# Kernel optimization log

Hardware: AMD Instinct MI355X
Metric: run time of the kernel (lower is better)

Reference implementation:

```python
import jax, jax.numpy as jnp
import numpy as np

N_NODES = 50000
N_EDGES = 800000
IN_CH, HID_CH, OUT_CH = 128, 256, 128


def _glorot(key, shape):
    fan_in, fan_out = shape[1], shape[0]
    lim = float(np.sqrt(6.0 / (fan_in + fan_out)))
    return jax.random.uniform(key, shape, jnp.float32, -lim, lim)


def setup_inputs() -> dict:
    key = jax.random.key(0)
    ks = jax.random.split(key, 8)
    x = jax.random.normal(ks[0], (N_NODES, IN_CH), jnp.float32)
    edge_index = jax.random.randint(ks[1], (2, N_EDGES), 0, N_NODES, jnp.int64)
    return {
        "x": x,
        "edge_index": edge_index,
        # layer 1: SAGEConv(128 -> 256): lin_l (with bias) on aggregated, lin_r (no bias) on root
        "W1l": _glorot(ks[2], (HID_CH, IN_CH)),
        "b1l": jnp.zeros((HID_CH,), jnp.float32),
        "W1r": _glorot(ks[3], (HID_CH, IN_CH)),
        # layer 2: SAGEConv(256 -> 128)
        "W2l": _glorot(ks[4], (OUT_CH, HID_CH)),
        "b2l": jnp.zeros((OUT_CH,), jnp.float32),
        "W2r": _glorot(ks[5], (OUT_CH, HID_CH)),
    }


def _sage_conv(x, src, dst, Wl, bl, Wr, n_nodes):
    # mean-aggregate neighbor (source) features at destination nodes
    msg = x[src]                                                   # [E, C] gather
    agg = jax.ops.segment_sum(msg, dst, num_segments=n_nodes)      # [N, C]
    deg = jax.ops.segment_sum(jnp.ones((src.shape[0],), x.dtype), dst,
                              num_segments=n_nodes)                # [N]
    mean = agg / jnp.maximum(deg, 1.0)[:, None]                    # zero-degree -> 0
    return mean @ Wl.T + bl + x @ Wr.T


def reference(x, edge_index, W1l, b1l, W1r, W2l, b2l, W2r):
    src, dst = edge_index[0], edge_index[1]
    n = x.shape[0]
    h = _sage_conv(x, src, dst, W1l, b1l, W1r, n)
    h = jax.nn.relu(h)  # dropout is identity in eval mode
    out = _sage_conv(h, src, dst, W2l, b2l, W2r, n)
    return out
```

## Files before the change

### kernel.cpp

```cpp
#include <hip/hip_runtime.h>

#define N_NODES 50000
#define IN_CH   128
#define HID_CH  256
#define OUT_CH  128

#define NB    196
#define NWG   256
#define NBNW  (NB * NWG)

#define XBLK  3125
#define WBLK  64

typedef __attribute__((ext_vector_type(8))) short bf16x8;
typedef __attribute__((ext_vector_type(4))) float f32x4;
typedef __attribute__((ext_vector_type(2))) float f32x2;

__device__ __forceinline__ unsigned short f32_bf16_rne(float f) {
    unsigned u = __float_as_uint(f);
    unsigned r = u + 0x7fff + ((u >> 16) & 1);
    return (unsigned short)(r >> 16);
}

__device__ __forceinline__ void cvt8_io(const float* __restrict__ inp,
                                        unsigned short* __restrict__ outp)
{
    const float4* p = reinterpret_cast<const float4*>(inp);
    float4 a = p[0], b = p[1];
    alignas(16) unsigned short t[8] = {
        f32_bf16_rne(a.x), f32_bf16_rne(a.y), f32_bf16_rne(a.z), f32_bf16_rne(a.w),
        f32_bf16_rne(b.x), f32_bf16_rne(b.y), f32_bf16_rne(b.z), f32_bf16_rne(b.w)};
    *reinterpret_cast<int4*>(outp) = *reinterpret_cast<const int4*>(t);
}

__global__ __launch_bounds__(256) void prep_kernel(
    const int* __restrict__ src, const int* __restrict__ dst,
    int* __restrict__ counts, int E, int chunk,
    const float* __restrict__ x, unsigned short* __restrict__ A1,
    unsigned char* __restrict__ xb8,
    const float* __restrict__ W1l, const float* __restrict__ W1r,
    const float* __restrict__ W2l, const float* __restrict__ W2r,
    unsigned short* __restrict__ B1, unsigned short* __restrict__ W2cat)
{
    const int b = blockIdx.x;
    if (b < NWG) {
        __shared__ int h[NB];
        for (int i = threadIdx.x; i < NB; i += 256) h[i] = 0;
        __syncthreads();
        const int e0 = b * chunk;
        const int e1 = min(e0 + chunk, E);
        for (int e = e0 + threadIdx.x; e < e1; e += 256) {
            int s = src[e], d = dst[e];
            if ((unsigned)s < (unsigned)N_NODES && (unsigned)d < (unsigned)N_NODES)
                atomicAdd(&h[d >> 8], 1);
        }
        __syncthreads();
        for (int i = threadIdx.x; i < NB; i += 256)
            counts[i * NWG + b] = h[i];
    } else if (b < NWG + XBLK) {
        size_t j = (size_t)(b - NWG) * 256 + threadIdx.x;
        const float4* p = reinterpret_cast<const float4*>(x) + 2 * j;
        float4 a = p[0], bb = p[1];
        alignas(16) unsigned short t[8] = {
            f32_bf16_rne(a.x),  f32_bf16_rne(a.y),  f32_bf16_rne(a.z),  f32_bf16_rne(a.w),
            f32_bf16_rne(bb.x), f32_bf16_rne(bb.y), f32_bf16_rne(bb.z), f32_bf16_rne(bb.w)};
        const size_t node = j >> 4, chunk16 = j & 15;
        *reinterpret_cast<int4*>(A1 + node * 256 + 128 + chunk16 * 8) =
            *reinterpret_cast<const int4*>(t);
        unsigned u0 = __builtin_amdgcn_cvt_pk_fp8_f32(a.x, a.y, 0, false);
        u0 = __builtin_amdgcn_cvt_pk_fp8_f32(a.z, a.w, u0, true);
        unsigned u1 = __builtin_amdgcn_cvt_pk_fp8_f32(bb.x, bb.y, 0, false);
        u1 = __builtin_amdgcn_cvt_pk_fp8_f32(bb.z, bb.w, u1, true);
        uint2 uv; uv.x = u0; uv.y = u1;
        *reinterpret_cast<uint2*>(xb8 + 8 * j) = uv;
    } else {
        int idx = (b - NWG - XBLK) * 256 + threadIdx.x;
        int seg = idx >> 12, j = idx & 4095;
        if (seg == 0) {
            int row = j >> 4, cb = (j & 15) * 8;
            cvt8_io(W1l + (size_t)j * 8, B1 + (size_t)row * 256 + cb);
        } else if (seg == 1) {
            int row = j >> 4, cb = (j & 15) * 8;
            cvt8_io(W1r + (size_t)j * 8, B1 + (size_t)row * 256 + 128 + cb);
        } else if (seg == 2) {
            int row = j >> 5, cb = (j & 31) * 8;
            cvt8_io(W2l + (size_t)j * 8, W2cat + (size_t)row * 256 + cb);
        } else {
            int row = j >> 5, cb = (j & 31) * 8;
            cvt8_io(W2r + (size_t)j * 8, W2cat + (size_t)(128 + row) * 256 + cb);
        }
    }
}

__global__ __launch_bounds__(256) void scan_kernel(
    const int* __restrict__ counts, int* __restrict__ S)
{
    __shared__ int red[256];
    const int t = threadIdx.x;
    const int b = blockIdx.x;
    const int lim = b * NWG;
    int partial = 0;
    for (int i = t; i < lim; i += 256) partial += counts[i];
    red[t] = partial;
    __syncthreads();
    for (int off = 128; off >= 1; off >>= 1) {
        if (t < off) red[t] += red[t + off];
        __syncthreads();
    }
    const int base_b = red[0];
    __syncthreads();
    const int v = counts[b * NWG + t];
    red[t] = v;
    __syncthreads();
    for (int off = 1; off < 256; off <<= 1) {
        int u = (t >= off) ? red[t - off] : 0;
        __syncthreads();
        if (t >= off) red[t] += u;
        __syncthreads();
    }
    S[b * NWG + t] = base_b + red[t] - v;
    if (b == NB - 1 && t == 255) S[NBNW] = base_b + red[255];
}

__global__ __launch_bounds__(256) void bscatter_kernel(
    const int* __restrict__ src, const int* __restrict__ dst,
    const int* __restrict__ S, int* __restrict__ pairs, int E, int chunk)
{
    __shared__ int cur[NB];
    const int w = blockIdx.x;
    for (int i = threadIdx.x; i < NB; i += 256) cur[i] = S[i * NWG + w];
    __syncthreads();
    const int e0 = w * chunk;
    const int e1 = min(e0 + chunk, E);
    for (int e = e0 + threadIdx.x; e < e1; e += 256) {
        int s = src[e], d = dst[e];
        if ((unsigned)s < (unsigned)N_NODES && (unsigned)d < (unsigned)N_NODES) {
            int pos = atomicAdd(&cur[d >> 8], 1);
            pairs[pos] = (s << 8) | (d & 255);
        }
    }
}

__global__ __launch_bounds__(256) void bsort_kernel(
    const int* __restrict__ pairs, const int* __restrict__ S,
    int* __restrict__ rowptr, int* __restrict__ colidx)
{
    __shared__ int hcnt[256];
    __shared__ int hcur[256];
    const int b = blockIdx.x;
    const int start = S[b * NWG];
    const int endv  = (b == NB - 1) ? S[NBNW] : S[(b + 1) * NWG];

    hcnt[threadIdx.x] = 0;
    __syncthreads();
    for (int e = start + threadIdx.x; e < endv; e += 256)
        atomicAdd(&hcnt[pairs[e] & 255], 1);
    __syncthreads();
    for (int off = 1; off < 256; off <<= 1) {
        int t = (threadIdx.x >= off) ? hcnt[threadIdx.x - off] : 0;
        __syncthreads();
        if (threadIdx.x >= off) hcnt[threadIdx.x] += t;
        __syncthreads();
    }
    int offv = (threadIdx.x == 0) ? 0 : hcnt[threadIdx.x - 1];
    hcur[threadIdx.x] = offv;
    int node = (b << 8) + threadIdx.x;
    if (node < N_NODES) rowptr[node] = start + offv;
    if (b == NB - 1 && threadIdx.x == 0) rowptr[N_NODES] = endv;
    __syncthreads();
    for (int e = start + threadIdx.x; e < endv; e += 256) {
        int p = pairs[e];
        int pos = atomicAdd(&hcur[p & 255], 1);
        colidx[start + pos] = (unsigned)p >> 8;
    }
}

#define ACC16(v)                                                             \
    { f32x2 a0 = __builtin_amdgcn_cvt_pk_f32_fp8(v.x, false);                \
      f32x2 a1 = __builtin_amdgcn_cvt_pk_f32_fp8(v.x, true);                 \
      f32x2 a2 = __builtin_amdgcn_cvt_pk_f32_fp8(v.y, false);                \
      f32x2 a3 = __builtin_amdgcn_cvt_pk_f32_fp8(v.y, true);                 \
      f32x2 a4 = __builtin_amdgcn_cvt_pk_f32_fp8(v.z, false);                \
      f32x2 a5 = __builtin_amdgcn_cvt_pk_f32_fp8(v.z, true);                 \
      f32x2 a6 = __builtin_amdgcn_cvt_pk_f32_fp8(v.w, false);                \
      f32x2 a7 = __builtin_amdgcn_cvt_pk_f32_fp8(v.w, true);                 \
      acc[0]  += a0.x; acc[1]  += a0.y; acc[2]  += a1.x; acc[3]  += a1.y;    \
      acc[4]  += a2.x; acc[5]  += a2.y; acc[6]  += a3.x; acc[7]  += a3.y;    \
      acc[8]  += a4.x; acc[9]  += a4.y; acc[10] += a5.x; acc[11] += a5.y;    \
      acc[12] += a6.x; acc[13] += a6.y; acc[14] += a7.x; acc[15] += a7.y; }

#define LDROW16(s, CH) (*reinterpret_cast<const uint4*>(feat + (size_t)(s) * (CH) + c16))

#define AGG_BODY(CH)                                                            \
    const int node = blockIdx.x * 16 + (threadIdx.x >> 4);                      \
    if (node >= N_NODES) return;                                                \
    const int l8 = threadIdx.x & 15;                                            \
    const int half = l8 >> 3;                  \
    const int c16 = (l8 & 7) * 16;                   \
    const int beg = rowptr[node], end = rowptr[node + 1];                       \
    const int len = end - beg;                                                  \
    float acc[16] = {};                                                         \
    for (int base = beg; base < end; base += 16) {                              \
        const int cnt = min(16, end - base);                                    \
        int ci = colidx[base + ((l8 < cnt) ? l8 : 0)];                          \
        int k = 0;                                                              \
        for (; k + 7 < cnt; k += 8) {                                           \
            int s0 = __shfl(ci, k + half,     16);                              \
            int s1 = __shfl(ci, k + half + 2, 16);                              \
            int s2 = __shfl(ci, k + half + 4, 16);                              \
            int s3 = __shfl(ci, k + half + 6, 16);                              \
            uint4 v0 = LDROW16(s0, CH); uint4 v1 = LDROW16(s1, CH);             \
            uint4 v2 = LDROW16(s2, CH); uint4 v3 = LDROW16(s3, CH);             \
            ACC16(v0) ACC16(v1) ACC16(v2) ACC16(v3)                             \
        }                                                                       \
        for (; k < cnt; k += 2) {                                               \
            int e = k + half;                                                   \
            int s0 = __shfl(ci, (e < cnt) ? e : 0, 16);                         \
            if (e < cnt) { uint4 v0 = LDROW16(s0, CH); ACC16(v0) }              \
        }                                                                       \
    }                                                                           \
    _Pragma("unroll")                                                           \
    for (int q = 0; q < 16; ++q) acc[q] += __shfl_xor(acc[q], 8);               \
    float accw[8];                                                              \
    _Pragma("unroll")                                                           \
    for (int q = 0; q < 8; ++q) accw[q] = half ? acc[q + 8] : acc[q];           \
    const int cb = c16 + half * 8;            \
    const float sc = 1.0f / fmaxf((float)len, 1.0f);

__global__ __launch_bounds__(256) void agg1_kernel(
    const unsigned char* __restrict__ feat, const int* __restrict__ rowptr,
    const int* __restrict__ colidx, unsigned short* __restrict__ A1)
{
    AGG_BODY(IN_CH)
    alignas(16) unsigned short t[8];
#pragma unroll
    for (int q = 0; q < 8; ++q) t[q] = f32_bf16_rne(accw[q] * sc);
    *reinterpret_cast<int4*>(A1 + (size_t)node * 256 + cb) =
        *reinterpret_cast<const int4*>(t);
}

__global__ __launch_bounds__(256) void agg2_kernel(
    const unsigned char* __restrict__ feat, const int* __restrict__ rowptr,
    const int* __restrict__ colidx, const unsigned short* __restrict__ hrb,
    const float* __restrict__ b2l, float* __restrict__ out)
{
    AGG_BODY(OUT_CH)
    const int4 hv = *reinterpret_cast<const int4*>(hrb + (size_t)node * OUT_CH + cb);
    const unsigned short* hs = reinterpret_cast<const unsigned short*>(&hv);
    float4 b0 = *reinterpret_cast<const float4*>(b2l + cb);
    float4 b1 = *reinterpret_cast<const float4*>(b2l + cb + 4);
    float4 o0, o1;
    o0.x = accw[0] * sc + __uint_as_float((unsigned)hs[0] << 16) + b0.x;
    o0.y = accw[1] * sc + __uint_as_float((unsigned)hs[1] << 16) + b0.y;
    o0.z = accw[2] * sc + __uint_as_float((unsigned)hs[2] << 16) + b0.z;
    o0.w = accw[3] * sc + __uint_as_float((unsigned)hs[3] << 16) + b0.w;
    o1.x = accw[4] * sc + __uint_as_float((unsigned)hs[4] << 16) + b1.x;
    o1.y = accw[5] * sc + __uint_as_float((unsigned)hs[5] << 16) + b1.y;
    o1.z = accw[6] * sc + __uint_as_float((unsigned)hs[6] << 16) + b1.z;
    o1.w = accw[7] * sc + __uint_as_float((unsigned)hs[7] << 16) + b1.w;
    float* o = out + (size_t)node * OUT_CH + cb;
    reinterpret_cast<float4*>(o)[0] = o0;
    reinterpret_cast<float4*>(o)[1] = o1;
}

template <int NIT>
__device__ __forceinline__ void stage8(
    const unsigned short* __restrict__ g, int ldg, int rowBase, int maxRow,
    int kBase, unsigned short* __restrict__ s, int tid)
{
    const int wave = tid >> 6;
    const int lane = tid & 63;
    const int r_in = lane >> 3;
    const int c_g  = (lane & 7) ^ r_in;
#pragma unroll
    for (int it = 0; it < NIT; ++it) {
        const int rowBlk = it * 64 + wave * 8;
        int row = rowBase + rowBlk + r_in;
        if (row >= maxRow) row = maxRow - 1;
        const unsigned short* gp = g + (size_t)row * ldg + kBase + c_g * 8;
        unsigned short* lp = s + rowBlk * 64;
        __builtin_amdgcn_global_load_lds(
            (const __attribute__((address_space(1))) unsigned int*)gp,
            (__attribute__((address_space(3))) unsigned int*)lp,
            16, 0, 0);
    }
}

__device__ __forceinline__ const bf16x8* frag_ptr(
    const unsigned short* __restrict__ s, int rr, int c)
{
    return reinterpret_cast<const bf16x8*>(s + rr * 64 + (((c ^ (rr & 7))) << 3));
}

__device__ __forceinline__ const bf16x8* hfrag_ptr(
    const unsigned short* __restrict__ s, int rr, int kbc, int c)
{
    return reinterpret_cast<const bf16x8*>(
        s + rr * 256 + ((kbc + (c ^ (rr & 7))) << 3));
}

__device__ __forceinline__ void mfma_tile(
    const unsigned short* __restrict__ As, const unsigned short* __restrict__ Bs,
    int wm, int wn, int l16, int quad, f32x4 acc[4][4])
{
#pragma unroll
    for (int k0 = 0; k0 < 64; k0 += 32) {
        const int c = (k0 >> 3) + quad;
        bf16x8 a[4], b[4];
#pragma unroll
        for (int i = 0; i < 4; ++i)
            a[i] = *frag_ptr(As, wm * 64 + i * 16 + l16, c);
#pragma unroll
        for (int j = 0; j < 4; ++j)
            b[j] = *frag_ptr(Bs, wn * 64 + j * 16 + l16, c);
#pragma unroll
        for (int i = 0; i < 4; ++i)
#pragma unroll
            for (int j = 0; j < 4; ++j)
                acc[i][j] = __builtin_amdgcn_mfma_f32_16x16x32_bf16(
                    b[j], a[i], acc[i][j], 0, 0, 0);
    }
}

__device__ __forceinline__ void mfma_tile_h(
    const unsigned short* __restrict__ Hs, const unsigned short* __restrict__ Bs,
    int kbc, int wm, int wn, int l16, int quad, f32x4 acc[4][4])
{
#pragma unroll
    for (int k0 = 0; k0 < 64; k0 += 32) {
        const int c = (k0 >> 3) + quad;
        bf16x8 a[4], b[4];
#pragma unroll
        for (int i = 0; i < 4; ++i)
            a[i] = *hfrag_ptr(Hs, wm * 64 + i * 16 + l16, kbc, c);
#pragma unroll
        for (int j = 0; j < 4; ++j)
            b[j] = *frag_ptr(Bs, wn * 64 + j * 16 + l16, c);
#pragma unroll
        for (int i = 0; i < 4; ++i)
#pragma unroll
            for (int j = 0; j < 4; ++j)
                acc[i][j] = __builtin_amdgcn_mfma_f32_16x16x32_bf16(
                    b[j], a[i], acc[i][j], 0, 0, 0);
    }
}

__global__ __launch_bounds__(512) void gemm_fused(
    const unsigned short* __restrict__ A1, const unsigned short* __restrict__ B1,
    const float* __restrict__ b1l, const unsigned short* __restrict__ W2cat,
    unsigned char* __restrict__ pb8, unsigned short* __restrict__ hrb)
{
    __shared__ unsigned short As[128 * 64];
    __shared__ unsigned short Bs[256 * 64];
    __shared__ unsigned short Hs[128 * 256];
    const int tid = threadIdx.x;
    const int wid = tid >> 6, lane = tid & 63;
    const int wm = wid & 1, wn = wid >> 1;
    const int l16 = lane & 15, quad = lane >> 4;
    const int rowBase = blockIdx.x * 128;

    f32x4 z = {0.f, 0.f, 0.f, 0.f};
    f32x4 acc[4][4];
#pragma unroll
    for (int i = 0; i < 4; ++i)
#pragma unroll
        for (int j = 0; j < 4; ++j) acc[i][j] = z;

#pragma unroll
    for (int kb = 0; kb < 256; kb += 64) {
        __syncthreads();
        stage8<2>(A1, 256, rowBase, N_NODES, kb, As, tid);
        stage8<4>(B1, 256, 0, HID_CH, kb, Bs, tid);
        __syncthreads();
        mfma_tile(As, Bs, wm, wn, l16, quad, acc);
    }

#pragma unroll
    for (int i = 0; i < 4; ++i) {
        const int rr = wm * 64 + i * 16 + l16;
#pragma unroll
        for (int j = 0; j < 4; ++j) {
            const int colBase = wn * 64 + j * 16 + quad * 4;
            float4 bv = *reinterpret_cast<const float4*>(b1l + colBase);
            alignas(8) unsigned short t[4];
            t[0] = f32_bf16_rne(fmaxf(acc[i][j][0] + bv.x, 0.0f));
            t[1] = f32_bf16_rne(fmaxf(acc[i][j][1] + bv.y, 0.0f));
            t[2] = f32_bf16_rne(fmaxf(acc[i][j][2] + bv.z, 0.0f));
            t[3] = f32_bf16_rne(fmaxf(acc[i][j][3] + bv.w, 0.0f));
            const int grp  = colBase >> 6;
            const int lc   = (colBase >> 3) & 7;
            const int half = (colBase >> 2) & 1;
            unsigned short* hp = Hs + rr * 256 +
                (((grp << 3) + (lc ^ (rr & 7))) << 3) + half * 4;
            *reinterpret_cast<uint2*>(hp) = *reinterpret_cast<const uint2*>(t);
        }
    }

#pragma unroll
    for (int i = 0; i < 4; ++i)
#pragma unroll
        for (int j = 0; j < 4; ++j) acc[i][j] = z;

#pragma unroll
    for (int kb = 0; kb < HID_CH; kb += 64) {
        __syncthreads();
        stage8<4>(W2cat, HID_CH, 0, 256, kb, Bs, tid);
        __syncthreads();
        mfma_tile_h(Hs, Bs, kb >> 3, wm, wn, l16, quad, acc);
    }

    if (wn < 2) {
#pragma unroll
        for (int i = 0; i < 4; ++i) {
            int m = rowBase + wm * 64 + i * 16 + l16;
            if (m >= N_NODES) continue;
#pragma unroll
            for (int j = 0; j < 4; ++j) {
                int col = wn * 64 + j * 16 + quad * 4;
                unsigned u = __builtin_amdgcn_cvt_pk_fp8_f32(
                    acc[i][j][0], acc[i][j][1], 0, false);
                u = __builtin_amdgcn_cvt_pk_fp8_f32(
                    acc[i][j][2], acc[i][j][3], u, true);
                *reinterpret_cast<unsigned*>(pb8 + (size_t)m * OUT_CH + col) = u;
            }
        }
    } else {
#pragma unroll
        for (int i = 0; i < 4; ++i) {
            int m = rowBase + wm * 64 + i * 16 + l16;
            if (m >= N_NODES) continue;
#pragma unroll
            for (int j = 0; j < 4; ++j) {
                int col = wn * 64 + j * 16 + quad * 4 - 128;
                alignas(8) unsigned short t[4];
                t[0] = f32_bf16_rne(acc[i][j][0]);
                t[1] = f32_bf16_rne(acc[i][j][1]);
                t[2] = f32_bf16_rne(acc[i][j][2]);
                t[3] = f32_bf16_rne(acc[i][j][3]);
                *reinterpret_cast<uint2*>(hrb + (size_t)m * OUT_CH + col) =
                    *reinterpret_cast<const uint2*>(t);
            }
        }
    }
}

extern "C" void kernel_launch(void* const* d_in, const int* in_sizes, int n_in,
                              void* d_out, int out_size, void* d_ws, size_t ws_size,
                              hipStream_t stream)
{
    const float* x   = (const float*)d_in[0];
    const int*   ei  = (const int*)d_in[1];
    const float* W1l = (const float*)d_in[2];
    const float* b1l = (const float*)d_in[3];
    const float* W1r = (const float*)d_in[4];
    const float* W2l = (const float*)d_in[5];
    const float* b2l = (const float*)d_in[6];
    const float* W2r = (const float*)d_in[7];

    const int E = in_sizes[1] / 2;
    const int* src = ei;
    const int* dst = ei + E;

    char* ws = (char*)d_ws;
    size_t off = 0;
    auto alloc = [&](size_t bytes) {
        void* p = ws + off;
        off += (bytes + 255) & ~(size_t)255;
        return p;
    };
    unsigned short* A1     = (unsigned short*)alloc((size_t)N_NODES * 256 * 2);
    unsigned char*  xb8    = (unsigned char*)alloc((size_t)N_NODES * IN_CH);
    unsigned char*  pb8    = (unsigned char*)alloc((size_t)N_NODES * OUT_CH);
    unsigned short* hrb    = (unsigned short*)alloc((size_t)N_NODES * OUT_CH * 2);
    unsigned short* B1     = (unsigned short*)alloc((size_t)HID_CH * 256 * 2);
    unsigned short* W2cat  = (unsigned short*)alloc((size_t)256 * HID_CH * 2);
    int* counts = (int*)alloc((size_t)NBNW * 4);
    int* S      = (int*)alloc((size_t)(NBNW + 1) * 4);
    int* pairs  = (int*)alloc((size_t)E * 4);
    int* rowptr = (int*)alloc((size_t)(N_NODES + 1) * 4);
    int* colidx = (int*)alloc((size_t)E * 4);
    float* out = (float*)d_out;

    const int chunk = (E + NWG - 1) / NWG;

    prep_kernel<<<NWG + XBLK + WBLK, 256, 0, stream>>>(
        src, dst, counts, E, chunk, x, A1, xb8,
        W1l, W1r, W2l, W2r, B1, W2cat);
    scan_kernel<<<NB, 256, 0, stream>>>(counts, S);
    bscatter_kernel<<<NWG, 256, 0, stream>>>(src, dst, S, pairs, E, chunk);
    bsort_kernel<<<NB, 256, 0, stream>>>(pairs, S, rowptr, colidx);

    const int aggBlocks = (N_NODES + 15) / 16;
    const int mBlocks = (N_NODES + 127) / 128;

    agg1_kernel<<<aggBlocks, 256, 0, stream>>>(xb8, rowptr, colidx, A1);
    gemm_fused<<<mBlocks, 512, 0, stream>>>(A1, B1, b1l, W2cat, pb8, hrb);
    agg2_kernel<<<aggBlocks, 256, 0, stream>>>(pb8, rowptr, colidx, hrb, b2l, out);
}
```

Before: 263.6 us.

## Use 8 lanes per node in aggregation with 8-edge unrolled gathers

The neighbor aggregation kernels now assign 8 lanes per node instead of 16. Each lane covers all 16 fp8 channels of a 16-byte chunk and processes every edge, rather than splitting edges across two half-groups. This removes the cross-half shuffle reduction and doubles the number of nodes per block. It also unrolls 8 independent row gathers per iteration to keep more loads in flight. In exchange, each lane does twice the serial accumulation work per node, which may lengthen latency for high-degree nodes.

```diff
diff --git a/kernel.cpp b/kernel.cpp
--- a/kernel.cpp
+++ b/kernel.cpp
@@ -189,54 +189,59 @@
       acc[8]  += a4.x; acc[9]  += a4.y; acc[10] += a5.x; acc[11] += a5.y;    \
       acc[12] += a6.x; acc[13] += a6.y; acc[14] += a7.x; acc[15] += a7.y; }
 
-#define LDROW16(s, CH) (*reinterpret_cast<const uint4*>(feat + (size_t)(s) * (CH) + c16))
-
-#define AGG_BODY(CH)                                                            \
-    const int node = blockIdx.x * 16 + (threadIdx.x >> 4);                      \
-    if (node >= N_NODES) return;                                                \
-    const int l8 = threadIdx.x & 15;                                            \
-    const int half = l8 >> 3;                  \
-    const int c16 = (l8 & 7) * 16;                   \
-    const int beg = rowptr[node], end = rowptr[node + 1];                       \
-    const int len = end - beg;                                                  \
+#define LDROW16(s, CH) (*reinterpret_cast<const uint4*>(feat + (size_t)(s) * (CH) + l8 * 16))
+
+#define AGG_LOOP(CH)                                                            \
     float acc[16] = {};                                                         \
-    for (int base = beg; base < end; base += 16) {                              \
-        const int cnt = min(16, end - base);                                    \
+    for (int base = beg; base < end; base += 8) {                               \
+        const int cnt = min(8, end - base);                                     \
         int ci = colidx[base + ((l8 < cnt) ? l8 : 0)];                          \
-        int k = 0;                                                              \
-        for (; k + 7 < cnt; k += 8) {                                           \
-            int s0 = __shfl(ci, k + half,     16);                              \
-            int s1 = __shfl(ci, k + half + 2, 16);                              \
-            int s2 = __shfl(ci, k + half + 4, 16);                              \
-            int s3 = __shfl(ci, k + half + 6, 16);                              \
+        if (cnt == 8) {                                                         \
+            int s0 = __shfl(ci, 0, 8), s1 = __shfl(ci, 1, 8);                   \
+            int s2 = __shfl(ci, 2, 8), s3 = __shfl(ci, 3, 8);                   \
+            int s4 = __shfl(ci, 4, 8), s5 = __shfl(ci, 5, 8);                   \
+            int s6 = __shfl(ci, 6, 8), s7 = __shfl(ci, 7, 8);                   \
             uint4 v0 = LDROW16(s0, CH); uint4 v1 = LDROW16(s1, CH);             \
             uint4 v2 = LDROW16(s2, CH); uint4 v3 = LDROW16(s3, CH);             \
+            uint4 v4 = LDROW16(s4, CH); uint4 v5 = LDROW16(s5, CH);             \
+            uint4 v6 = LDROW16(s6, CH); uint4 v7 = LDROW16(s7, CH);             \
             ACC16(v0) ACC16(v1) ACC16(v2) ACC16(v3)                             \
-        }                                                                       \
-        for (; k < cnt; k += 2) {                                               \
-            int e = k + half;                                                   \
-            int s0 = __shfl(ci, (e < cnt) ? e : 0, 16);                         \
-            if (e < cnt) { uint4 v0 = LDROW16(s0, CH); ACC16(v0) }              \
+            ACC16(v4) ACC16(v5) ACC16(v6) ACC16(v7)                             \
+        } else {                                                                \
+            int k = 0;                                                          \
+            if (cnt >= 4) {                                                     \
+                int s0 = __shfl(ci, 0, 8), s1 = __shfl(ci, 1, 8);               \
+                int s2 = __shfl(ci, 2, 8), s3 = __shfl(ci, 3, 8);               \
+                uint4 v0 = LDROW16(s0, CH); uint4 v1 = LDROW16(s1, CH);         \
+                uint4 v2 = LDROW16(s2, CH); uint4 v3 = LDROW16(s3, CH);         \
+                ACC16(v0) ACC16(v1) ACC16(v2) ACC16(v3)                         \
+                k = 4;                                                          \
+            }                                                                   \
+            for (; k < cnt; ++k) {                                              \
+                int s0 = __shfl(ci, k, 8);                                      \
+                uint4 v0 = LDROW16(s0, CH);                                     \
+                ACC16(v0)                                                       \
+            }                                                                   \
         }                                                                       \
     }                                                                           \
-    _Pragma("unroll")                                                           \
-    for (int q = 0; q < 16; ++q) acc[q] += __shfl_xor(acc[q], 8);               \
-    float accw[8];                                                              \
-    _Pragma("unroll")                                                           \
-    for (int q = 0; q < 8; ++q) accw[q] = half ? acc[q + 8] : acc[q];           \
-    const int cb = c16 + half * 8;            \
     const float sc = 1.0f / fmaxf((float)len, 1.0f);
 
 __global__ __launch_bounds__(256) void agg1_kernel(
     const unsigned char* __restrict__ feat, const int* __restrict__ rowptr,
     const int* __restrict__ colidx, unsigned short* __restrict__ A1)
 {
-    AGG_BODY(IN_CH)
-    alignas(16) unsigned short t[8];
-#pragma unroll
-    for (int q = 0; q < 8; ++q) t[q] = f32_bf16_rne(accw[q] * sc);
-    *reinterpret_cast<int4*>(A1 + (size_t)node * 256 + cb) =
-        *reinterpret_cast<const int4*>(t);
+    const int node = blockIdx.x * 32 + (threadIdx.x >> 3);
+    if (node >= N_NODES) return;
+    const int l8 = threadIdx.x & 7;
+    const int beg = rowptr[node], end = rowptr[node + 1];
+    const int len = end - beg;
+    AGG_LOOP(IN_CH)
+    alignas(16) unsigned short t[16];
+#pragma unroll
+    for (int q = 0; q < 16; ++q) t[q] = f32_bf16_rne(acc[q] * sc);
+    int4* dstp = reinterpret_cast<int4*>(A1 + (size_t)node * 256 + l8 * 16);
+    dstp[0] = reinterpret_cast<const int4*>(t)[0];
+    dstp[1] = reinterpret_cast<const int4*>(t)[1];
 }
 
 __global__ __launch_bounds__(256) void agg2_kernel(
@@ -244,23 +249,29 @@
     const int* __restrict__ colidx, const unsigned short* __restrict__ hrb,
     const float* __restrict__ b2l, float* __restrict__ out)
 {
-    AGG_BODY(OUT_CH)
-    const int4 hv = *reinterpret_cast<const int4*>(hrb + (size_t)node * OUT_CH + cb);
-    const unsigned short* hs = reinterpret_cast<const unsigned short*>(&hv);
-    float4 b0 = *reinterpret_cast<const float4*>(b2l + cb);
-    float4 b1 = *reinterpret_cast<const float4*>(b2l + cb + 4);
-    float4 o0, o1;
-    o0.x = accw[0] * sc + __uint_as_float((unsigned)hs[0] << 16) + b0.x;
-    o0.y = accw[1] * sc + __uint_as_float((unsigned)hs[1] << 16) + b0.y;
-    o0.z = accw[2] * sc + __uint_as_float((unsigned)hs[2] << 16) + b0.z;
-    o0.w = accw[3] * sc + __uint_as_float((unsigned)hs[3] << 16) + b0.w;
-    o1.x = accw[4] * sc + __uint_as_float((unsigned)hs[4] << 16) + b1.x;
-    o1.y = accw[5] * sc + __uint_as_float((unsigned)hs[5] << 16) + b1.y;
-    o1.z = accw[6] * sc + __uint_as_float((unsigned)hs[6] << 16) + b1.z;
-    o1.w = accw[7] * sc + __uint_as_float((unsigned)hs[7] << 16) + b1.w;
-    float* o = out + (size_t)node * OUT_CH + cb;
-    reinterpret_cast<float4*>(o)[0] = o0;
-    reinterpret_cast<float4*>(o)[1] = o1;
+    const int node = blockIdx.x * 32 + (threadIdx.x >> 3);
+    if (node >= N_NODES) return;
+    const int l8 = threadIdx.x & 7;
+    const int beg = rowptr[node], end = rowptr[node + 1];
+    const int len = end - beg;
+    AGG_LOOP(OUT_CH)
+    const unsigned short* hp = hrb + (size_t)node * OUT_CH + l8 * 16;
+    const int4 hv0 = reinterpret_cast<const int4*>(hp)[0];
+    const int4 hv1 = reinterpret_cast<const int4*>(hp)[1];
+    const unsigned short* hs0 = reinterpret_cast<const unsigned short*>(&hv0);
+    const unsigned short* hs1 = reinterpret_cast<const unsigned short*>(&hv1);
+    const float* bb = b2l + l8 * 16;
+    alignas(16) float tv[16];
+#pragma unroll
+    for (int q = 0; q < 8; ++q)
+        tv[q] = acc[q] * sc + __uint_as_float((unsigned)hs0[q] << 16) + bb[q];
+#pragma unroll
+    for (int q = 0; q < 8; ++q)
+        tv[q + 8] = acc[q + 8] * sc + __uint_as_float((unsigned)hs1[q] << 16) + bb[q + 8];
+    float* o = out + (size_t)node * OUT_CH + l8 * 16;
+#pragma unroll
+    for (int q = 0; q < 4; ++q)
+        reinterpret_cast<float4*>(o)[q] = reinterpret_cast<const float4*>(tv)[q];
 }
 
 template <int NIT>
@@ -490,7 +501,7 @@
     bscatter_kernel<<<NWG, 256, 0, stream>>>(src, dst, S, pairs, E, chunk);
     bsort_kernel<<<NB, 256, 0, stream>>>(pairs, S, rowptr, colidx);
 
-    const int aggBlocks = (N_NODES + 15) / 16;
+    const int aggBlocks = (N_NODES + 31) / 32;
     const int mBlocks = (N_NODES + 127) / 128;
 
     agg1_kernel<<<aggBlocks, 256, 0, stream>>>(xb8, rowptr, colidx, A1);
```

Measured after the change: 225.2 us. -14.6%, faster.
